# Optimization experiments

Measured on AMD Instinct MI355X. Metric: run time of the kernel, lower is better.

Reference implementation:

```python
import jax, jax.numpy as jnp
import numpy as np

BN_EPS = 1e-5


def setup_inputs() -> dict:
    key = jax.random.key(0)
    ks = jax.random.split(key, 8)
    B, C1, H, W = 8, 256, 128, 128
    C2 = 512
    mid = max(1, (C1 * 3) // 16)  # 48
    x = jax.random.normal(ks[0], (B, C1, H, W), dtype=jnp.float32)
    w1 = jax.random.normal(ks[1], (mid, C1 * 3), dtype=jnp.float32) * 0.05
    w2 = jax.random.normal(ks[2], (C1 * 3, mid), dtype=jnp.float32) * 0.05
    conv_w = jax.random.normal(ks[3], (C2, C1 * 4), dtype=jnp.float32) * 0.03
    bn_gamma = jnp.ones((C2,), dtype=jnp.float32)
    bn_beta = jnp.zeros((C2,), dtype=jnp.float32)
    bn_mean = jax.random.normal(ks[4], (C2,), dtype=jnp.float32)
    bn_var = jax.random.uniform(ks[5], (C2,), dtype=jnp.float32)
    return {"x": x, "w1": w1, "w2": w2, "conv_w": conv_w,
            "bn_gamma": bn_gamma, "bn_beta": bn_beta,
            "bn_mean": bn_mean, "bn_var": bn_var}


def reference(x, w1, w2, conv_w, bn_gamma, bn_beta, bn_mean, bn_var):
    B, C, H, W = x.shape
    # Depthwise 2x2 stride-2 Haar conv == linear combos of the 2x2 pixel blocks.
    x00 = x[:, :, 0::2, 0::2]
    x01 = x[:, :, 0::2, 1::2]
    x10 = x[:, :, 1::2, 0::2]
    x11 = x[:, :, 1::2, 1::2]
    # filters: LL=lo(kh)lo(kw), LH=hi(kh)lo(kw), HL=lo(kh)hi(kw), HH=hi*hi
    # with reversed haar taps lo=[s,s], hi=[s,-s], s=1/sqrt(2); s^2 = 0.5
    LL = 0.5 * (x00 + x01 + x10 + x11)
    LH = 0.5 * (x00 + x01 - x10 - x11)
    HL = 0.5 * (x00 - x01 + x10 - x11)
    HH = 0.5 * (x00 - x01 - x10 + x11)
    H2, W2 = H // 2, W // 2
    # interleaved per-channel order [c0_LH,c0_HL,c0_HH,c1_LH,...], matching
    # out.view(B,C,4,...)[:, :, 1:].view(B, 3C, ...)
    hf = jnp.stack([LH, HL, HH], axis=2).reshape(B, 3 * C, H2, W2)
    # SE channel attention on high-frequency bands
    y = hf.mean(axis=(2, 3))                       # [B, 3C]
    y = jax.nn.relu(y @ w1.T)                      # [B, mid]
    y = jax.nn.sigmoid(y @ w2.T)                   # [B, 3C]
    hf = hf * y[:, :, None, None]
    fused = jnp.concatenate([LL, hf], axis=1)      # [B, 4C, H2, W2]
    # 1x1 conv (bias-free) + BN (eval mode, running stats) + SiLU
    z = jnp.einsum('bchw,oc->bohw', fused, conv_w)
    inv = jax.lax.rsqrt(bn_var + BN_EPS)
    z = (z - bn_mean[None, :, None, None]) * (bn_gamma * inv)[None, :, None, None] \
        + bn_beta[None, :, None, None]
    return z * jax.nn.sigmoid(z)
```

## Files before the change

kernel.cpp:

```cpp
#include <hip/hip_runtime.h>
#include <stdint.h>

#define B_    8
#define C1_   256
#define H_    128
#define W_    128
#define H2_   64
#define HW_   4096
#define KDIM  1024
#define C2_   512
#define MID_  48
#define CHF_  768

typedef __attribute__((ext_vector_type(8))) short short8;
typedef __attribute__((ext_vector_type(4))) float f32x4;

__device__ __forceinline__ unsigned short f2bf(float f) {
  unsigned int u = __float_as_uint(f);
  u += 0x7fffu + ((u >> 16) & 1u);
  return (unsigned short)(u >> 16);
}
__device__ __forceinline__ float bf2f(unsigned short h) {
  return __uint_as_float(((unsigned int)h) << 16);
}

__global__ __launch_bounds__(256) void k1_wavelet(const float* __restrict__ x,
                                                  unsigned short* __restrict__ fused_t,
                                                  float* __restrict__ chanSums) {
  __shared__ unsigned short ll_s[64 * 66];
  __shared__ unsigned short hf_s[64 * 198];
  const int tid = threadIdx.x;
  const int h2 = blockIdx.x;
  const int b  = blockIdx.y;
  const int w2 = tid & 63;
  const int cg = tid >> 6;
  const float* xb = x + (size_t)b * C1_ * H_ * W_;
  const size_t rowbase = ((size_t)b * HW_ + (size_t)h2 * 64) * KDIM;

  for (int q = 0; q < 4; ++q) {
#pragma unroll 4
    for (int i = 0; i < 16; ++i) {
      int cl = cg * 16 + i;
      int c  = q * 64 + cl;
      const float* xp = xb + (size_t)c * (H_ * W_) + (2 * h2) * W_ + 2 * w2;
      float2 r0 = *(const float2*)xp;
      float2 r1 = *(const float2*)(xp + W_);
      float x00 = r0.x, x01 = r0.y, x10 = r1.x, x11 = r1.y;
      float LL = 0.5f * (x00 + x01 + x10 + x11);
      float LH = 0.5f * (x00 + x01 - x10 - x11);
      float HL = 0.5f * (x00 - x01 + x10 - x11);
      float HH = 0.5f * (x00 - x01 - x10 + x11);
      ll_s[w2 * 66 + cl]          = f2bf(LL);
      hf_s[w2 * 198 + 3 * cl + 0] = f2bf(LH);
      hf_s[w2 * 198 + 3 * cl + 1] = f2bf(HL);
      hf_s[w2 * 198 + 3 * cl + 2] = f2bf(HH);
    }
    __syncthreads();
    {
      const unsigned int* lw = (const unsigned int*)ll_s;
#pragma unroll
      for (int t = 0; t < 8; ++t) {
        int idx = t * 256 + tid;
        int row = idx >> 5, w = idx & 31;
        unsigned int v = lw[row * 33 + w];
        *(unsigned int*)((char*)(fused_t + rowbase + (size_t)row * KDIM + q * 64) + w * 4) = v;
      }
    }
    {
      const unsigned int* hv = (const unsigned int*)hf_s;
#pragma unroll
      for (int t = 0; t < 24; ++t) {
        int idx = t * 256 + tid;
        int row = idx / 96, w = idx - row * 96;
        unsigned int v = hv[row * 99 + w];
        *(unsigned int*)((char*)(fused_t + rowbase + (size_t)row * KDIM + 256 + q * 192) + w * 4) = v;
      }
    }
    if (tid < 192) {
      float s = 0.f;
#pragma unroll 8
      for (int r = 0; r < 64; ++r) s += bf2f(hf_s[r * 198 + tid]);
      atomicAdd(&chanSums[b * CHF_ + q * 192 + tid], s);
    }
    __syncthreads();
  }
}

__global__ __launch_bounds__(256) void k2_mlp(const float* __restrict__ chanSums,
                                              const float* __restrict__ w1,
                                              const float* __restrict__ w2,
                                              const float* __restrict__ gamma,
                                              const float* __restrict__ beta,
                                              const float* __restrict__ mean,
                                              const float* __restrict__ var,
                                              float* __restrict__ scaleArr,
                                              float* __restrict__ bnA,
                                              float* __restrict__ bnB) {
  __shared__ float mean_s[CHF_];
  __shared__ float part_s[192];
  __shared__ float y1_s[MID_];
  const int tid = threadIdx.x;
  const int b = blockIdx.x;
  for (int k = tid; k < CHF_; k += 256)
    mean_s[k] = chanSums[b * CHF_ + k] * (1.0f / 4096.0f);
  __syncthreads();
  if (tid < 192) {
    int m = tid >> 2, p = tid & 3;
    const float* wr = w1 + (size_t)m * CHF_ + p * 192;
    const float* ms = mean_s + p * 192;
    float s = 0.f;
#pragma unroll 8
    for (int k = 0; k < 192; ++k) s += ms[k] * wr[k];
    part_s[tid] = s;
  }
  __syncthreads();
  if (tid < MID_) {
    float s = part_s[4 * tid] + part_s[4 * tid + 1] + part_s[4 * tid + 2] + part_s[4 * tid + 3];
    y1_s[tid] = fmaxf(s, 0.f);
  }
  __syncthreads();
  for (int c = tid; c < CHF_; c += 256) {
    const float* wr = w2 + (size_t)c * MID_;
    float d = 0.f;
#pragma unroll
    for (int m = 0; m < MID_; ++m) d += y1_s[m] * wr[m];
    scaleArr[b * KDIM + 256 + c] = 1.0f / (1.0f + __expf(-d));
  }
  scaleArr[b * KDIM + tid] = 1.0f;
  if (b == 0) {
    for (int o = tid; o < C2_; o += 256) {
      float inv = rsqrtf(var[o] + 1e-5f);
      float a = gamma[o] * inv;
      bnA[o] = a;
      bnB[o] = beta[o] - mean[o] * a;
    }
  }
}

__global__ __launch_bounds__(256) void k2b_scalew(const float* __restrict__ conv_w,
                                                  const float* __restrict__ scaleArr,
                                                  unsigned short* __restrict__ conv_ws) {
  int idx = blockIdx.x * 256 + threadIdx.x;
  int b = idx >> 17;
  int rem = idx & 131071;
  int o = rem >> 8;
  int c = (rem & 255) * 4;
  float4 wv = *(const float4*)(conv_w + (size_t)o * KDIM + c);
  float4 sv = *(const float4*)(scaleArr + b * KDIM + c);
  ushort4 r;
  r.x = f2bf(wv.x * sv.x);
  r.y = f2bf(wv.y * sv.y);
  r.z = f2bf(wv.z * sv.z);
  r.w = f2bf(wv.w * sv.w);
  *(ushort4*)(conv_ws + ((size_t)(b * C2_ + o) * KDIM + c)) = r;
}

typedef const __attribute__((address_space(1))) unsigned int* gas_u32p;
typedef __attribute__((address_space(3))) unsigned int* las_u32p;
__device__ __forceinline__ void async_ld16(const void* g, void* l) {
  __builtin_amdgcn_global_load_lds((gas_u32p)g, (las_u32p)l, 16, 0, 0);
}

__global__ __launch_bounds__(256, 2) void k3_gemm(const unsigned short* __restrict__ conv_ws,
                                                  const unsigned short* __restrict__ fused_t,
                                                  const float* __restrict__ bnA,
                                                  const float* __restrict__ bnB,
                                                  float* __restrict__ out) {
  __shared__ short As[128 * 32];
  __shared__ short Bs[128 * 32];
  const int tid  = threadIdx.x;
  const int lane = tid & 63;
  const int wave = tid >> 6;
  const int b  = blockIdx.z;
  const int m0 = blockIdx.y * 128;
  const int n0 = blockIdx.x * 128;
  const char* Abase = (const char*)(conv_ws + (size_t)b * C2_ * KDIM);
  const char* Bbase = (const char*)(fused_t + (size_t)b * HW_ * KDIM);
  const int srow = wave * 32 + (lane >> 2);
  const int kb   = (lane & 3) * 16;
  const char* gA = Abase + (size_t)(m0 + srow) * (KDIM * 2) + kb;
  const char* gB = Bbase + (size_t)(n0 + srow) * (KDIM * 2) + kb;
  short* lA0 = As + (wave * 32) * 32;
  short* lA1 = As + (wave * 32 + 16) * 32;
  short* lB0 = Bs + (wave * 32) * 32;
  short* lB1 = Bs + (wave * 32 + 16) * 32;
  const int wm = wave & 1, wn = wave >> 1;
  const int frow = lane & 15;
  const int koff = (lane >> 4) * 8;
  f32x4 acc[4][4] = {};

  for (int k0 = 0; k0 < KDIM; k0 += 32) {
    async_ld16(gA,                   lA0);
    async_ld16(gA + 16 * (KDIM * 2), lA1);
    async_ld16(gB,                   lB0);
    async_ld16(gB + 16 * (KDIM * 2), lB1);
    gA += 64; gB += 64;
    __syncthreads();
    short8 af[4], bf[4];
#pragma unroll
    for (int im = 0; im < 4; ++im)
      af[im] = *(const short8*)(As + (wm * 64 + im * 16 + frow) * 32 + koff);
#pragma unroll
    for (int in = 0; in < 4; ++in)
      bf[in] = *(const short8*)(Bs + (wn * 64 + in * 16 + frow) * 32 + koff);
#pragma unroll
    for (int im = 0; im < 4; ++im)
#pragma unroll
      for (int in = 0; in < 4; ++in)
        acc[im][in] = __builtin_amdgcn_mfma_f32_16x16x32_bf16(af[im], bf[in], acc[im][in], 0, 0, 0);
    __syncthreads();
  }

  float* outb = out + (size_t)b * C2_ * HW_;
#pragma unroll
  for (int im = 0; im < 4; ++im) {
    int obase = m0 + wm * 64 + im * 16 + (lane >> 4) * 4;
#pragma unroll
    for (int r = 0; r < 4; ++r) {
      int o = obase + r;
      float a = bnA[o], c0 = bnB[o];
#pragma unroll
      for (int in = 0; in < 4; ++in) {
        int hw = n0 + wn * 64 + in * 16 + (lane & 15);
        float z = acc[im][in][r] * a + c0;
        outb[(size_t)o * HW_ + hw] = z / (1.0f + __expf(-z));
      }
    }
  }
}

extern "C" void kernel_launch(void* const* d_in, const int* in_sizes, int n_in,
                              void* d_out, int out_size, void* d_ws, size_t ws_size,
                              hipStream_t stream) {
  const float* x      = (const float*)d_in[0];
  const float* w1     = (const float*)d_in[1];
  const float* w2     = (const float*)d_in[2];
  const float* conv_w = (const float*)d_in[3];
  const float* gamma  = (const float*)d_in[4];
  const float* beta   = (const float*)d_in[5];
  const float* mean   = (const float*)d_in[6];
  const float* var    = (const float*)d_in[7];
  float* out = (float*)d_out;

  char* ws = (char*)d_ws;
  unsigned short* fused_t = (unsigned short*)ws;
  unsigned short* conv_ws = (unsigned short*)(ws + (size_t)67108864);
  float* chanSums = (float*)(ws + (size_t)75497472);
  float* scaleArr = (float*)(ws + (size_t)75522048);
  float* bnA      = (float*)(ws + (size_t)75554816);
  float* bnB      = (float*)(ws + (size_t)75556864);

  hipMemsetAsync(chanSums, 0, B_ * CHF_ * sizeof(float), stream);
  k1_wavelet<<<dim3(64, 8), 256, 0, stream>>>(x, fused_t, chanSums);
  k2_mlp<<<dim3(8), 256, 0, stream>>>(chanSums, w1, w2, gamma, beta, mean, var,
                                      scaleArr, bnA, bnB);
  k2b_scalew<<<dim3(4096), 256, 0, stream>>>(conv_w, scaleArr, conv_ws);
  k3_gemm<<<dim3(32, 4, 8), 256, 0, stream>>>(conv_ws, fused_t, bnA, bnB, out);
}
```

Before: 302.1 us.

## Switch GEMM to 32x32x16 MFMA with K=64 swizzled tiles, vectorize wavelet loads

The GEMM now uses 32x32x16 bf16 MFMA with 2x2 accumulators per wave and a K-step of 64, staged in XOR-swizzled LDS tiles to avoid bank conflicts. The point is to halve the barriers per K and raise MFMA efficiency. The wavelet kernel loads float4 so each thread covers two output pixels. The atomic channel sums and their memset are replaced by per-row partial sums that the MLP kernel reduces. LDS use per block doubles, and the epilogue stores are now strided differently.

```diff
diff --git a/kernel.cpp b/kernel.cpp
--- a/kernel.cpp
+++ b/kernel.cpp
@@ -13,7 +13,7 @@
 #define CHF_  768
 
 typedef __attribute__((ext_vector_type(8))) short short8;
-typedef __attribute__((ext_vector_type(4))) float f32x4;
+typedef __attribute__((ext_vector_type(16))) float f32x16;
 
 __device__ __forceinline__ unsigned short f2bf(float f) {
   unsigned int u = __float_as_uint(f);
@@ -32,28 +32,43 @@
   const int tid = threadIdx.x;
   const int h2 = blockIdx.x;
   const int b  = blockIdx.y;
-  const int w2 = tid & 63;
-  const int cg = tid >> 6;
+  const int w4 = tid & 31;
+  const int grp = tid >> 5;
   const float* xb = x + (size_t)b * C1_ * H_ * W_;
   const size_t rowbase = ((size_t)b * HW_ + (size_t)h2 * 64) * KDIM;
 
   for (int q = 0; q < 4; ++q) {
-#pragma unroll 4
-    for (int i = 0; i < 16; ++i) {
-      int cl = cg * 16 + i;
+#pragma unroll
+    for (int i = 0; i < 8; ++i) {
+      int cl = grp * 8 + i;
       int c  = q * 64 + cl;
-      const float* xp = xb + (size_t)c * (H_ * W_) + (2 * h2) * W_ + 2 * w2;
-      float2 r0 = *(const float2*)xp;
-      float2 r1 = *(const float2*)(xp + W_);
-      float x00 = r0.x, x01 = r0.y, x10 = r1.x, x11 = r1.y;
-      float LL = 0.5f * (x00 + x01 + x10 + x11);
-      float LH = 0.5f * (x00 + x01 - x10 - x11);
-      float HL = 0.5f * (x00 - x01 + x10 - x11);
-      float HH = 0.5f * (x00 - x01 - x10 + x11);
-      ll_s[w2 * 66 + cl]          = f2bf(LL);
-      hf_s[w2 * 198 + 3 * cl + 0] = f2bf(LH);
-      hf_s[w2 * 198 + 3 * cl + 1] = f2bf(HL);
-      hf_s[w2 * 198 + 3 * cl + 2] = f2bf(HH);
+      const float* xp = xb + (size_t)c * (H_ * W_) + (2 * h2) * W_ + 4 * w4;
+      float4 r0 = *(const float4*)xp;
+      float4 r1 = *(const float4*)(xp + W_);
+      {
+        float x00 = r0.x, x01 = r0.y, x10 = r1.x, x11 = r1.y;
+        float LL = 0.5f * (x00 + x01 + x10 + x11);
+        float LH = 0.5f * (x00 + x01 - x10 - x11);
+        float HL = 0.5f * (x00 - x01 + x10 - x11);
+        float HH = 0.5f * (x00 - x01 - x10 + x11);
+        int w2 = 2 * w4;
+        ll_s[w2 * 66 + cl]          = f2bf(LL);
+        hf_s[w2 * 198 + 3 * cl + 0] = f2bf(LH);
+        hf_s[w2 * 198 + 3 * cl + 1] = f2bf(HL);
+        hf_s[w2 * 198 + 3 * cl + 2] = f2bf(HH);
+      }
+      {
+        float x00 = r0.z, x01 = r0.w, x10 = r1.z, x11 = r1.w;
+        float LL = 0.5f * (x00 + x01 + x10 + x11);
+        float LH = 0.5f * (x00 + x01 - x10 - x11);
+        float HL = 0.5f * (x00 - x01 + x10 - x11);
+        float HH = 0.5f * (x00 - x01 - x10 + x11);
+        int w2 = 2 * w4 + 1;
+        ll_s[w2 * 66 + cl]          = f2bf(LL);
+        hf_s[w2 * 198 + 3 * cl + 0] = f2bf(LH);
+        hf_s[w2 * 198 + 3 * cl + 1] = f2bf(HL);
+        hf_s[w2 * 198 + 3 * cl + 2] = f2bf(HH);
+      }
     }
     __syncthreads();
     {
@@ -80,7 +95,7 @@
       float s = 0.f;
 #pragma unroll 8
       for (int r = 0; r < 64; ++r) s += bf2f(hf_s[r * 198 + tid]);
-      atomicAdd(&chanSums[b * CHF_ + q * 192 + tid], s);
+      chanSums[((size_t)(b * 64 + h2)) * CHF_ + q * 192 + tid] = s;
     }
     __syncthreads();
   }
@@ -101,8 +116,13 @@
   __shared__ float y1_s[MID_];
   const int tid = threadIdx.x;
   const int b = blockIdx.x;
-  for (int k = tid; k < CHF_; k += 256)
-    mean_s[k] = chanSums[b * CHF_ + k] * (1.0f / 4096.0f);
+  for (int k = tid; k < CHF_; k += 256) {
+    float s = 0.f;
+#pragma unroll 8
+    for (int h2 = 0; h2 < 64; ++h2)
+      s += chanSums[((size_t)(b * 64 + h2)) * CHF_ + k];
+    mean_s[k] = s * (1.0f / 4096.0f);
+  }
   __syncthreads();
   if (tid < 192) {
     int m = tid >> 2, p = tid & 3;
@@ -166,8 +186,8 @@
                                                   const float* __restrict__ bnA,
                                                   const float* __restrict__ bnB,
                                                   float* __restrict__ out) {
-  __shared__ short As[128 * 32];
-  __shared__ short Bs[128 * 32];
+  __shared__ short As[128 * 64];
+  __shared__ short Bs[128 * 64];
   const int tid  = threadIdx.x;
   const int lane = tid & 63;
   const int wave = tid >> 6;
@@ -176,53 +196,58 @@
   const int n0 = blockIdx.x * 128;
   const char* Abase = (const char*)(conv_ws + (size_t)b * C2_ * KDIM);
   const char* Bbase = (const char*)(fused_t + (size_t)b * HW_ * KDIM);
-  const int srow = wave * 32 + (lane >> 2);
-  const int kb   = (lane & 3) * 16;
-  const char* gA = Abase + (size_t)(m0 + srow) * (KDIM * 2) + kb;
-  const char* gB = Bbase + (size_t)(n0 + srow) * (KDIM * 2) + kb;
-  short* lA0 = As + (wave * 32) * 32;
-  short* lA1 = As + (wave * 32 + 16) * 32;
-  short* lB0 = Bs + (wave * 32) * 32;
-  short* lB1 = Bs + (wave * 32 + 16) * 32;
+  const int rloc = lane >> 3;
+  const int kb   = lane & 7;
+  const int kbsw = kb ^ rloc;
+  const char* gA = Abase + (size_t)(m0 + wave * 32 + rloc) * (KDIM * 2) + kbsw * 16;
+  const char* gB = Bbase + (size_t)(n0 + wave * 32 + rloc) * (KDIM * 2) + kbsw * 16;
+  short* lA = As + (wave * 32) * 64;
+  short* lB = Bs + (wave * 32) * 64;
   const int wm = wave & 1, wn = wave >> 1;
-  const int frow = lane & 15;
-  const int koff = (lane >> 4) * 8;
-  f32x4 acc[4][4] = {};
-
-  for (int k0 = 0; k0 < KDIM; k0 += 32) {
-    async_ld16(gA,                   lA0);
-    async_ld16(gA + 16 * (KDIM * 2), lA1);
-    async_ld16(gB,                   lB0);
-    async_ld16(gB + 16 * (KDIM * 2), lB1);
-    gA += 64; gB += 64;
-    __syncthreads();
-    short8 af[4], bf[4];
-#pragma unroll
-    for (int im = 0; im < 4; ++im)
-      af[im] = *(const short8*)(As + (wm * 64 + im * 16 + frow) * 32 + koff);
-#pragma unroll
-    for (int in = 0; in < 4; ++in)
-      bf[in] = *(const short8*)(Bs + (wn * 64 + in * 16 + frow) * 32 + koff);
-#pragma unroll
-    for (int im = 0; im < 4; ++im)
-#pragma unroll
-      for (int in = 0; in < 4; ++in)
-        acc[im][in] = __builtin_amdgcn_mfma_f32_16x16x32_bf16(af[im], bf[in], acc[im][in], 0, 0, 0);
+  const int r  = lane & 31;
+  const int hi = lane >> 5;
+  const int sw = r & 7;
+  f32x16 acc[2][2] = {};
+
+  for (int k0 = 0; k0 < KDIM; k0 += 64) {
+#pragma unroll
+    for (int t = 0; t < 4; ++t) {
+      async_ld16(gA + (size_t)t * 8 * (KDIM * 2), lA + t * 8 * 64);
+      async_ld16(gB + (size_t)t * 8 * (KDIM * 2), lB + t * 8 * 64);
+    }
+    gA += 128; gB += 128;
+    __syncthreads();
+#pragma unroll
+    for (int ks = 0; ks < 4; ++ks) {
+      const int kbg = 2 * ks + hi;
+      const int ko  = (kbg ^ sw) << 3;
+      short8 af[2], bf[2];
+#pragma unroll
+      for (int im = 0; im < 2; ++im)
+        af[im] = *(const short8*)(As + (wm * 64 + im * 32 + r) * 64 + ko);
+#pragma unroll
+      for (int in = 0; in < 2; ++in)
+        bf[in] = *(const short8*)(Bs + (wn * 64 + in * 32 + r) * 64 + ko);
+#pragma unroll
+      for (int im = 0; im < 2; ++im)
+#pragma unroll
+        for (int in = 0; in < 2; ++in)
+          acc[im][in] = __builtin_amdgcn_mfma_f32_32x32x16_bf16(af[im], bf[in], acc[im][in], 0, 0, 0);
+    }
     __syncthreads();
   }
 
   float* outb = out + (size_t)b * C2_ * HW_;
 #pragma unroll
-  for (int im = 0; im < 4; ++im) {
-    int obase = m0 + wm * 64 + im * 16 + (lane >> 4) * 4;
-#pragma unroll
-    for (int r = 0; r < 4; ++r) {
-      int o = obase + r;
-      float a = bnA[o], c0 = bnB[o];
-#pragma unroll
-      for (int in = 0; in < 4; ++in) {
-        int hw = n0 + wn * 64 + in * 16 + (lane & 15);
-        float z = acc[im][in][r] * a + c0;
+  for (int im = 0; im < 2; ++im) {
+#pragma unroll
+    for (int in = 0; in < 2; ++in) {
+      int hw = n0 + wn * 64 + in * 32 + r;
+#pragma unroll
+      for (int reg = 0; reg < 16; ++reg) {
+        int o = m0 + wm * 64 + im * 32 + (reg & 3) + 8 * (reg >> 2) + 4 * hi;
+        float a = bnA[o], c0 = bnB[o];
+        float z = acc[im][in][reg] * a + c0;
         outb[(size_t)o * HW_ + hw] = z / (1.0f + __expf(-z));
       }
     }
@@ -246,11 +271,10 @@
   unsigned short* fused_t = (unsigned short*)ws;
   unsigned short* conv_ws = (unsigned short*)(ws + (size_t)67108864);
   float* chanSums = (float*)(ws + (size_t)75497472);
-  float* scaleArr = (float*)(ws + (size_t)75522048);
-  float* bnA      = (float*)(ws + (size_t)75554816);
-  float* bnB      = (float*)(ws + (size_t)75556864);
-
-  hipMemsetAsync(chanSums, 0, B_ * CHF_ * sizeof(float), stream);
+  float* scaleArr = (float*)(ws + (size_t)77070336);
+  float* bnA      = (float*)(ws + (size_t)77103104);
+  float* bnB      = (float*)(ws + (size_t)77105152);
+
   k1_wavelet<<<dim3(64, 8), 256, 0, stream>>>(x, fused_t, chanSums);
   k2_mlp<<<dim3(8), 256, 0, stream>>>(chanSums, w1, w2, gamma, beta, mean, var,
                                       scaleArr, bnA, bnB);
```

After: 313.3 us. 1.04x slower.
